# Kernel optimization log

Hardware: AMD Instinct MI355X
Metric: run time of the kernel (lower is better)

The kernel has to match this reference:

```python
import jax, jax.numpy as jnp
import numpy as np

B = 16384          # batch_size / n_samples
SRC = 200          # source_num
C = 10             # category_size
I = SRC * C        # input_size = 2000
EPS = 1e-10


def setup_inputs() -> dict:
    key = jax.random.key(0)
    ks = jax.random.split(key, 8)
    # forward data
    x = jax.random.uniform(ks[0], (B, I), dtype=jnp.float32)
    mask = jax.random.uniform(ks[1], (B, I), dtype=jnp.float32)
    y_target = jax.random.uniform(ks[2], (B, C), dtype=jnp.float32)
    # learned parameters (xavier-uniform style init)
    def xavier(k, shape):
        fan_in, fan_out = shape[0], shape[1]
        limit = float(np.sqrt(2.0)) * float(np.sqrt(6.0 / (fan_in + fan_out)))
        return jax.random.uniform(k, shape, dtype=jnp.float32, minval=-limit, maxval=limit)
    W_reconstr = xavier(ks[3], (C, I))
    b_reconstr = xavier(ks[4], (1, I))
    W_yc = xavier(ks[5], (I, C))
    b_yc = xavier(ks[6], (1, C))
    return {"x": x, "mask": mask, "y_target": y_target,
            "W_reconstr": W_reconstr, "b_reconstr": b_reconstr,
            "W_yc": W_yc, "b_yc": b_yc}


def reference(x, mask, y_target, W_reconstr, b_reconstr, W_yc, b_yc):
    # ---- decoder (collapsed): constant_y[i] is a batch of identical one-hot
    # rows at category i, so y @ W_reconstr + b == W_reconstr[i] + b for all
    # batch elements. Stack over all i -> logits [C, I].
    logits = W_reconstr + b_reconstr                      # [C, I]
    e = jnp.exp(logits).reshape(C, SRC, C)                # per-source blocks
    # block-diagonal matmul == segmented sum over each source's C entries
    p = (e / e.sum(axis=-1, keepdims=True)).reshape(C, I)  # [C, I]
    logp = jnp.log(EPS + p)                               # [C, I]
    # -mean_j(mask * x * log p_i) per category i -> [B, C]
    reconstr_x = -(x * mask) @ logp.T / I

    # ---- encoder
    y_classifier = jax.nn.softmax(x @ W_yc + b_yc, axis=1)  # [B, C]

    # ---- losses
    loss_w_l1 = jnp.sum(jnp.abs(W_yc))
    loss_classifier_y_x = jnp.mean(jnp.sum(y_classifier * reconstr_x, axis=1))
    loss_y_kl = jnp.mean(jnp.sum(
        y_classifier * (jnp.log(EPS + y_classifier) - jnp.log(EPS + y_target)),
        axis=1))
    loss = (loss_classifier_y_x + 1e-4 * loss_y_kl
            + 0.005 / SRC / C / C * loss_w_l1)
    return (y_classifier, loss)
```

## Files before the change

### kernel.cpp

```cpp
#include <hip/hip_runtime.h>
#include <hip/hip_bf16.h>

#define B_SZ 16384
#define SRCN 200
#define CAT  10
#define IN   2000
#define KPAD 2048
#define EPSF 1e-10f

typedef short  short8 __attribute__((ext_vector_type(8)));
typedef float  f32x4  __attribute__((ext_vector_type(4)));

__device__ __forceinline__ short f2bf(float f) {
    union { float f; unsigned u; } v; v.f = f;
    unsigned r = (v.u + 0x7fffu + ((v.u >> 16) & 1u)) >> 16;
    return (short)r;
}

__global__ void prep_kernel(const float* __restrict__ W_rec,
                            const float* __restrict__ b_rec,
                            const float* __restrict__ W_yc,
                            short* __restrict__ logp_t,
                            short* __restrict__ wyc_t,
                            double* __restrict__ acc) {
    if (blockIdx.x == gridDim.x - 1) {
        float p = 0.f;
        for (int i = threadIdx.x; i < IN * CAT; i += blockDim.x) p += fabsf(W_yc[i]);
        __shared__ float red[4];
        for (int o = 32; o; o >>= 1) p += __shfl_down(p, o, 64);
        if ((threadIdx.x & 63) == 0) red[threadIdx.x >> 6] = p;
        __syncthreads();
        if (threadIdx.x == 0) {
            acc[0] = 0.0;
            acc[1] = 0.0;
            acc[2] = (double)(red[0] + red[1] + red[2] + red[3]);
        }
        return;
    }
    int tid = blockIdx.x * blockDim.x + threadIdx.x;
    int n = tid >> 11;
    int k = tid & 2047;
    short wv = 0, lv = 0;
    if (n < CAT && k < IN) {
        wv = f2bf(W_yc[k * CAT + n]);
        int base = (k / CAT) * CAT;
        float lg[CAT];
        float m = -1e30f;
        #pragma unroll
        for (int i = 0; i < CAT; i++) {
            lg[i] = W_rec[n * IN + base + i] + b_rec[base + i];
            m = fmaxf(m, lg[i]);
        }
        float s = 0.f;
        #pragma unroll
        for (int i = 0; i < CAT; i++) s += expf(lg[i] - m);
        float myl = W_rec[n * IN + k] + b_rec[k];
        float pp = expf(myl - m) / s;
        lv = f2bf(logf(EPSF + pp));
    }
    wyc_t[n * KPAD + k] = wv;
    logp_t[n * KPAD + k] = lv;
}

__global__ __launch_bounds__(512) void main_kernel(
        const float* __restrict__ x, const float* __restrict__ mask,
        const float* __restrict__ y_target, const float* __restrict__ b_yc,
        const short* __restrict__ logp_t, const short* __restrict__ wyc_t,
        float* __restrict__ out, double* __restrict__ acc) {
    const int l   = threadIdx.x & 63;
    const int w   = threadIdx.x >> 6;
    const int r0  = blockIdx.x * 16;
    const int m16 = l & 15;
    const int kg  = l >> 4;

    f32x4 accR = {0.f, 0.f, 0.f, 0.f};
    f32x4 accY = {0.f, 0.f, 0.f, 0.f};

    const size_t xbase = (size_t)(r0 + m16) * IN;
    const short* lpB = logp_t + m16 * KPAD;
    const short* wyB = wyc_t + m16 * KPAD;

    #pragma unroll 4
    for (int t = 0; t < 8; ++t) {
        const int kt = w * 8 + t;
        const int k0 = kt * 32 + kg * 8;
        const int kc = (k0 + 8 <= IN) ? k0 : 0;
        const float4* xp = reinterpret_cast<const float4*>(x + xbase + kc);
        const float4* mp = reinterpret_cast<const float4*>(mask + xbase + kc);
        float4 xa = xp[0], xb = xp[1];
        float4 ma = mp[0], mb = mp[1];
        float xs[8] = {xa.x, xa.y, xa.z, xa.w, xb.x, xb.y, xb.z, xb.w};
        float ms[8] = {ma.x, ma.y, ma.z, ma.w, mb.x, mb.y, mb.z, mb.w};
        short8 fx, fxm;
        #pragma unroll
        for (int e = 0; e < 8; e++) {
            fx[e]  = f2bf(xs[e]);
            fxm[e] = f2bf(xs[e] * ms[e]);
        }
        const short8 bR = *reinterpret_cast<const short8*>(lpB + k0);
        const short8 bW = *reinterpret_cast<const short8*>(wyB + k0);
        accR = __builtin_amdgcn_mfma_f32_16x16x32_bf16(fxm, bR, accR, 0, 0, 0);
        accY = __builtin_amdgcn_mfma_f32_16x16x32_bf16(fx,  bW, accY, 0, 0, 0);
    }

    __shared__ float lds[8][64][9];
    #pragma unroll
    for (int q = 0; q < 4; q++) {
        lds[w][l][q]     = accR[q];
        lds[w][l][4 + q] = accY[q];
    }
    __syncthreads();
    if (w != 0) return;
    f32x4 sR = {0.f, 0.f, 0.f, 0.f};
    f32x4 sY = {0.f, 0.f, 0.f, 0.f};
    #pragma unroll
    for (int w2 = 0; w2 < 8; w2++) {
        #pragma unroll
        for (int q = 0; q < 4; q++) {
            sR[q] += lds[w2][l][q];
            sY[q] += lds[w2][l][4 + q];
        }
    }

    const bool valid = (m16 < CAT);
    const float byc = valid ? b_yc[m16] : 0.f;
    float a_cls = 0.f, a_kl = 0.f;
    #pragma unroll
    for (int q = 0; q < 4; q++) {
        const int grow = r0 + kg * 4 + q;
        float z = sY[q] + byc;
        float zz = valid ? z : -1e30f;
        #pragma unroll
        for (int o = 1; o < 16; o <<= 1) zz = fmaxf(zz, __shfl_xor(zz, o, 64));
        float e = valid ? __expf(z - zz) : 0.f;
        float s = e;
        #pragma unroll
        for (int o = 1; o < 16; o <<= 1) s += __shfl_xor(s, o, 64);
        float y = e / s;
        float recon = -sR[q] * (1.f / IN);
        float cls = y * recon;
        float kl = 0.f;
        if (valid) {
            float yt = y_target[(size_t)grow * CAT + m16];
            kl = y * (logf(EPSF + y) - logf(EPSF + yt));
            out[(size_t)grow * CAT + m16] = y;
        }
        #pragma unroll
        for (int o = 1; o < 16; o <<= 1) {
            cls += __shfl_xor(cls, o, 64);
            kl  += __shfl_xor(kl, o, 64);
        }
        if (m16 == 0) { a_cls += cls; a_kl += kl; }
    }
    float vc = (m16 == 0) ? a_cls : 0.f;
    float vk = (m16 == 0) ? a_kl  : 0.f;
    vc += __shfl_xor(vc, 16, 64); vc += __shfl_xor(vc, 32, 64);
    vk += __shfl_xor(vk, 16, 64); vk += __shfl_xor(vk, 32, 64);
    if (l == 0) {
        atomicAdd(&acc[0], (double)vc);
        atomicAdd(&acc[1], (double)vk);
    }
}

__global__ void final_kernel(const double* __restrict__ acc,
                             float* __restrict__ out) {
    if (threadIdx.x == 0) {
        double loss = acc[0] / (double)B_SZ
                    + 1e-4 * (acc[1] / (double)B_SZ)
                    + (0.005 / (double)SRCN / (double)CAT / (double)CAT) * acc[2];
        out[(size_t)B_SZ * CAT] = (float)loss;
    }
}

extern "C" void kernel_launch(void* const* d_in, const int* in_sizes, int n_in,
                              void* d_out, int out_size, void* d_ws, size_t ws_size,
                              hipStream_t stream) {
    const float* x        = (const float*)d_in[0];
    const float* mask     = (const float*)d_in[1];
    const float* y_target = (const float*)d_in[2];
    const float* W_rec    = (const float*)d_in[3];
    const float* b_rec    = (const float*)d_in[4];
    const float* W_yc     = (const float*)d_in[5];
    const float* b_yc     = (const float*)d_in[6];
    float* out  = (float*)d_out;
    double* acc = (double*)d_ws;
    short* logp_t = (short*)((char*)d_ws + 256);
    short* wyc_t  = logp_t + 16 * KPAD;

    prep_kernel<<<129, 256, 0, stream>>>(W_rec, b_rec, W_yc, logp_t, wyc_t, acc);
    main_kernel<<<1024, 512, 0, stream>>>(x, mask, y_target, b_yc,
                                          logp_t, wyc_t, out, acc);
    final_kernel<<<1, 64, 0, stream>>>(acc, out);
}
```

Before: 85.36 us.

## Stage x and mask rows through swizzled LDS with coalesced row-wide loads

Each block now loads full rows of x and mask in 512-column chunks. Every wave reads contiguous 1KB spans, converts them to bf16 (plain and masked), and writes them into an XOR-swizzled shared-memory tile. The MFMA A-fragments are then read back from LDS. The goal is more coalesced global loads for the memory-bound input stream. The cost is extra LDS traffic and two barriers per chunk, with no double buffering, which may reduce how many loads are in flight. The launch bounds also gain a minimum-blocks hint, and the reduction buffer reuses the staging LDS.

New measurement: 85.31 us. Within noise of the previous version (-0.1%).

```diff
diff --git a/kernel.cpp b/kernel.cpp
--- a/kernel.cpp
+++ b/kernel.cpp
@@ -6,15 +6,23 @@
 #define CAT  10
 #define IN   2000
 #define KPAD 2048
+#define CHUNK 512
+#define NCH   4
+#define TSZ   16384
 #define EPSF 1e-10f
 
 typedef short  short8 __attribute__((ext_vector_type(8)));
+typedef short  short4v __attribute__((ext_vector_type(4)));
 typedef float  f32x4  __attribute__((ext_vector_type(4)));
 
 __device__ __forceinline__ short f2bf(float f) {
     union { float f; unsigned u; } v; v.f = f;
     unsigned r = (v.u + 0x7fffu + ((v.u >> 16) & 1u)) >> 16;
     return (short)r;
+}
+
+__device__ __forceinline__ int swz(int row, int colByte) {
+    return row * 1024 + (colByte ^ ((row & 7) << 4));
 }
 
 __global__ void prep_kernel(const float* __restrict__ W_rec,
@@ -62,11 +70,13 @@
     logp_t[n * KPAD + k] = lv;
 }
 
-__global__ __launch_bounds__(512) void main_kernel(
+__global__ __launch_bounds__(512, 8) void main_kernel(
         const float* __restrict__ x, const float* __restrict__ mask,
         const float* __restrict__ y_target, const float* __restrict__ b_yc,
         const short* __restrict__ logp_t, const short* __restrict__ wyc_t,
         float* __restrict__ out, double* __restrict__ acc) {
+    __shared__ __attribute__((aligned(16))) char smem[2 * TSZ];
+
     const int l   = threadIdx.x & 63;
     const int w   = threadIdx.x >> 6;
     const int r0  = blockIdx.x * 16;
@@ -76,38 +86,60 @@
     f32x4 accR = {0.f, 0.f, 0.f, 0.f};
     f32x4 accY = {0.f, 0.f, 0.f, 0.f};
 
-    const size_t xbase = (size_t)(r0 + m16) * IN;
     const short* lpB = logp_t + m16 * KPAD;
     const short* wyB = wyc_t + m16 * KPAD;
 
-    #pragma unroll 4
-    for (int t = 0; t < 8; ++t) {
-        const int kt = w * 8 + t;
-        const int k0 = kt * 32 + kg * 8;
-        const int kc = (k0 + 8 <= IN) ? k0 : 0;
-        const float4* xp = reinterpret_cast<const float4*>(x + xbase + kc);
-        const float4* mp = reinterpret_cast<const float4*>(mask + xbase + kc);
-        float4 xa = xp[0], xb = xp[1];
-        float4 ma = mp[0], mb = mp[1];
-        float xs[8] = {xa.x, xa.y, xa.z, xa.w, xb.x, xb.y, xb.z, xb.w};
-        float ms[8] = {ma.x, ma.y, ma.z, ma.w, mb.x, mb.y, mb.z, mb.w};
-        short8 fx, fxm;
-        #pragma unroll
-        for (int e = 0; e < 8; e++) {
-            fx[e]  = f2bf(xs[e]);
-            fxm[e] = f2bf(xs[e] * ms[e]);
-        }
-        const short8 bR = *reinterpret_cast<const short8*>(lpB + k0);
-        const short8 bW = *reinterpret_cast<const short8*>(wyB + k0);
-        accR = __builtin_amdgcn_mfma_f32_16x16x32_bf16(fxm, bR, accR, 0, 0, 0);
-        accY = __builtin_amdgcn_mfma_f32_16x16x32_bf16(fx,  bW, accY, 0, 0, 0);
-    }
-
-    __shared__ float lds[8][64][9];
+    for (int c = 0; c < NCH; ++c) {
+        #pragma unroll
+        for (int r = 0; r < 2; ++r) {
+            const int row = w + r * 8;
+            const size_t gb = (size_t)(r0 + row) * IN;
+            const int col0 = c * CHUNK + l * 4;
+            const int col1 = col0 + 256;
+            const bool ok0 = (col0 + 3) < IN;
+            const bool ok1 = (col1 + 3) < IN;
+            const float4 x0 = *reinterpret_cast<const float4*>(x + gb + (ok0 ? col0 : 0));
+            const float4 m0 = *reinterpret_cast<const float4*>(mask + gb + (ok0 ? col0 : 0));
+            const float4 x1 = *reinterpret_cast<const float4*>(x + gb + (ok1 ? col1 : 0));
+            const float4 m1 = *reinterpret_cast<const float4*>(mask + gb + (ok1 ? col1 : 0));
+            float xf[8] = {x0.x, x0.y, x0.z, x0.w, x1.x, x1.y, x1.z, x1.w};
+            float mf[8] = {m0.x, m0.y, m0.z, m0.w, m1.x, m1.y, m1.z, m1.w};
+            short4v xb0, xb1, xm0, xm1;
+            #pragma unroll
+            for (int e = 0; e < 4; ++e) {
+                float a0 = ok0 ? xf[e]     : 0.f;
+                float a1 = ok1 ? xf[4 + e] : 0.f;
+                xb0[e] = f2bf(a0);
+                xb1[e] = f2bf(a1);
+                xm0[e] = f2bf(a0 * mf[e]);
+                xm1[e] = f2bf(a1 * mf[4 + e]);
+            }
+            *reinterpret_cast<short4v*>(smem + swz(row, l * 8))             = xb0;
+            *reinterpret_cast<short4v*>(smem + swz(row, 512 + l * 8))       = xb1;
+            *reinterpret_cast<short4v*>(smem + TSZ + swz(row, l * 8))       = xm0;
+            *reinterpret_cast<short4v*>(smem + TSZ + swz(row, 512 + l * 8)) = xm1;
+        }
+        __syncthreads();
+
+        #pragma unroll
+        for (int t = 0; t < 2; ++t) {
+            const int kl = w * 64 + t * 32 + kg * 8;
+            const int kglob = c * CHUNK + kl;
+            const short8 aX  = *reinterpret_cast<const short8*>(smem + swz(m16, kl * 2));
+            const short8 aXM = *reinterpret_cast<const short8*>(smem + TSZ + swz(m16, kl * 2));
+            const short8 bRv = *reinterpret_cast<const short8*>(lpB + kglob);
+            const short8 bWv = *reinterpret_cast<const short8*>(wyB + kglob);
+            accR = __builtin_amdgcn_mfma_f32_16x16x32_bf16(aXM, bRv, accR, 0, 0, 0);
+            accY = __builtin_amdgcn_mfma_f32_16x16x32_bf16(aX,  bWv, accY, 0, 0, 0);
+        }
+        __syncthreads();
+    }
+
+    float (*red)[64][9] = reinterpret_cast<float (*)[64][9]>(smem);
     #pragma unroll
     for (int q = 0; q < 4; q++) {
-        lds[w][l][q]     = accR[q];
-        lds[w][l][4 + q] = accY[q];
+        red[w][l][q]     = accR[q];
+        red[w][l][4 + q] = accY[q];
     }
     __syncthreads();
     if (w != 0) return;
@@ -117,8 +149,8 @@
     for (int w2 = 0; w2 < 8; w2++) {
         #pragma unroll
         for (int q = 0; q < 4; q++) {
-            sR[q] += lds[w2][l][q];
-            sY[q] += lds[w2][l][4 + q];
+            sR[q] += red[w2][l][q];
+            sY[q] += red[w2][l][4 + q];
         }
     }
 
```

## Double-buffer x/mask tiles into LDS via async global_load_lds with swizzle

Applied to the files above, without the earlier changes.

Rewrites the main kernel so x and mask chunks stream directly from global memory into swizzled LDS buffers using global_load_lds. Two buffers are used, and the chunk c+2 loads overlap with MFMA compute on the current chunk. The bf16 weight operands are preloaded into registers up front, and the block shrinks to 256 threads with occupancy 2. The aim is to hide HBM latency on this bandwidth-bound read of x and mask. The cost is heavy register use for the preloaded weights, explicit waitcnt and barrier synchronisation, and reliance on zero-padded weights to cancel the clamped out-of-range loads.

New measurement: 80.33 us. -5.9%, faster.

```diff
diff --git a/kernel.cpp b/kernel.cpp
--- a/kernel.cpp
+++ b/kernel.cpp
@@ -6,6 +6,11 @@
 #define CAT  10
 #define IN   2000
 #define KPAD 2048
+#define CHUNKF 256
+#define NCH   8
+#define ROWB  1024
+#define TBUF  16384
+#define BUFSZ 32768
 #define EPSF 1e-10f
 
 typedef short  short8 __attribute__((ext_vector_type(8)));
@@ -15,6 +20,13 @@
     union { float f; unsigned u; } v; v.f = f;
     unsigned r = (v.u + 0x7fffu + ((v.u >> 16) & 1u)) >> 16;
     return (short)r;
+}
+
+__device__ __forceinline__ void gload16(const void* g, void* l) {
+    __builtin_amdgcn_global_load_lds(
+        (const __attribute__((address_space(1))) void*)g,
+        (__attribute__((address_space(3))) void*)l,
+        16, 0, 0);
 }
 
 __global__ void prep_kernel(const float* __restrict__ W_rec,
@@ -62,63 +74,102 @@
     logp_t[n * KPAD + k] = lv;
 }
 
-__global__ __launch_bounds__(512) void main_kernel(
+__global__ __launch_bounds__(256, 2) void main_kernel(
         const float* __restrict__ x, const float* __restrict__ mask,
         const float* __restrict__ y_target, const float* __restrict__ b_yc,
         const short* __restrict__ logp_t, const short* __restrict__ wyc_t,
         float* __restrict__ out, double* __restrict__ acc) {
+    __shared__ __attribute__((aligned(16))) char smem[2 * BUFSZ];
+
     const int l   = threadIdx.x & 63;
     const int w   = threadIdx.x >> 6;
     const int r0  = blockIdx.x * 16;
     const int m16 = l & 15;
     const int kg  = l >> 4;
 
+    const short* lpB = logp_t + m16 * KPAD;
+    const short* wyB = wyc_t + m16 * KPAD;
+
+    short8 bR[NCH][2], bW[NCH][2];
+    #pragma unroll
+    for (int c = 0; c < NCH; ++c) {
+        #pragma unroll
+        for (int t = 0; t < 2; ++t) {
+            const int kglob = c * CHUNKF + w * 64 + t * 32 + kg * 8;
+            bR[c][t] = *reinterpret_cast<const short8*>(lpB + kglob);
+            bW[c][t] = *reinterpret_cast<const short8*>(wyB + kglob);
+        }
+    }
+
     f32x4 accR = {0.f, 0.f, 0.f, 0.f};
     f32x4 accY = {0.f, 0.f, 0.f, 0.f};
 
-    const size_t xbase = (size_t)(r0 + m16) * IN;
-    const short* lpB = logp_t + m16 * KPAD;
-    const short* wyB = wyc_t + m16 * KPAD;
-
-    #pragma unroll 4
-    for (int t = 0; t < 8; ++t) {
-        const int kt = w * 8 + t;
-        const int k0 = kt * 32 + kg * 8;
-        const int kc = (k0 + 8 <= IN) ? k0 : 0;
-        const float4* xp = reinterpret_cast<const float4*>(x + xbase + kc);
-        const float4* mp = reinterpret_cast<const float4*>(mask + xbase + kc);
-        float4 xa = xp[0], xb = xp[1];
-        float4 ma = mp[0], mb = mp[1];
-        float xs[8] = {xa.x, xa.y, xa.z, xa.w, xb.x, xb.y, xb.z, xb.w};
-        float ms[8] = {ma.x, ma.y, ma.z, ma.w, mb.x, mb.y, mb.z, mb.w};
-        short8 fx, fxm;
-        #pragma unroll
-        for (int e = 0; e < 8; e++) {
-            fx[e]  = f2bf(xs[e]);
-            fxm[e] = f2bf(xs[e] * ms[e]);
-        }
-        const short8 bR = *reinterpret_cast<const short8*>(lpB + k0);
-        const short8 bW = *reinterpret_cast<const short8*>(wyB + k0);
-        accR = __builtin_amdgcn_mfma_f32_16x16x32_bf16(fxm, bR, accR, 0, 0, 0);
-        accY = __builtin_amdgcn_mfma_f32_16x16x32_bf16(fx,  bW, accY, 0, 0, 0);
-    }
-
-    __shared__ float lds[8][64][9];
+    auto stage = [&](int c, int b) {
+        #pragma unroll
+        for (int i = 0; i < 4; ++i) {
+            const int lr = w * 4 + i;
+            const size_t gb = (size_t)(r0 + lr) * IN;
+            int srcf = c * CHUNKF + ((l ^ (lr & 7)) << 2);
+            if (srcf > IN - 4) srcf = IN - 4;
+            gload16(x + gb + srcf,    smem + b * BUFSZ + lr * ROWB);
+            gload16(mask + gb + srcf, smem + b * BUFSZ + TBUF + lr * ROWB);
+        }
+    };
+
+    auto compute = [&](int c) {
+        const char* base = smem + (c & 1) * BUFSZ;
+        const int swzk = (m16 & 7) << 4;
+        #pragma unroll
+        for (int t = 0; t < 2; ++t) {
+            const int kl = w * 64 + t * 32 + kg * 8;
+            const int a0 = m16 * ROWB + ((kl * 4) ^ swzk);
+            const int a1 = a0 ^ 16;
+            f32x4 x0 = *reinterpret_cast<const f32x4*>(base + a0);
+            f32x4 x1 = *reinterpret_cast<const f32x4*>(base + a1);
+            f32x4 m0 = *reinterpret_cast<const f32x4*>(base + TBUF + a0);
+            f32x4 m1 = *reinterpret_cast<const f32x4*>(base + TBUF + a1);
+            short8 fx, fxm;
+            #pragma unroll
+            for (int e = 0; e < 4; ++e) {
+                fx[e]      = f2bf(x0[e]);
+                fx[4 + e]  = f2bf(x1[e]);
+                fxm[e]     = f2bf(x0[e] * m0[e]);
+                fxm[4 + e] = f2bf(x1[e] * m1[e]);
+            }
+            accR = __builtin_amdgcn_mfma_f32_16x16x32_bf16(fxm, bR[c][t], accR, 0, 0, 0);
+            accY = __builtin_amdgcn_mfma_f32_16x16x32_bf16(fx,  bW[c][t], accY, 0, 0, 0);
+        }
+    };
+
+    stage(0, 0);
+    stage(1, 1);
+    #pragma unroll
+    for (int c = 0; c < NCH; ++c) {
+        if (c < NCH - 1) { asm volatile("s_waitcnt vmcnt(8)" ::: "memory"); }
+        else             { asm volatile("s_waitcnt vmcnt(0)" ::: "memory"); }
+        __builtin_amdgcn_s_barrier();
+        compute(c);
+        asm volatile("s_waitcnt lgkmcnt(0)" ::: "memory");
+        __builtin_amdgcn_s_barrier();
+        if (c + 2 < NCH) stage(c + 2, c & 1);
+    }
+
+    float (*red)[64][9] = reinterpret_cast<float (*)[64][9]>(smem);
     #pragma unroll
     for (int q = 0; q < 4; q++) {
-        lds[w][l][q]     = accR[q];
-        lds[w][l][4 + q] = accY[q];
+        red[w][l][q]     = accR[q];
+        red[w][l][4 + q] = accY[q];
     }
     __syncthreads();
     if (w != 0) return;
     f32x4 sR = {0.f, 0.f, 0.f, 0.f};
     f32x4 sY = {0.f, 0.f, 0.f, 0.f};
     #pragma unroll
-    for (int w2 = 0; w2 < 8; w2++) {
+    for (int w2 = 0; w2 < 4; w2++) {
         #pragma unroll
         for (int q = 0; q < 4; q++) {
-            sR[q] += lds[w2][l][q];
-            sY[q] += lds[w2][l][4 + q];
+            sR[q] += red[w2][l][q];
+            sY[q] += red[w2][l][4 + q];
         }
     }
 
@@ -188,7 +239,7 @@
     short* wyc_t  = logp_t + 16 * KPAD;
 
     prep_kernel<<<129, 256, 0, stream>>>(W_rec, b_rec, W_yc, logp_t, wyc_t, acc);
-    main_kernel<<<1024, 512, 0, stream>>>(x, mask, y_target, b_yc,
+    main_kernel<<<1024, 256, 0, stream>>>(x, mask, y_target, b_yc,
                                           logp_t, wyc_t, out, acc);
     final_kernel<<<1, 64, 0, stream>>>(acc, out);
 }
```
